# Kernel optimization log

Measured on AMD Instinct MI355X. Metric: run time of the kernel, lower is better.

Reference implementation:

```python
import jax, jax.numpy as jnp
import numpy as np


def _gcn_layer(h, src, dst, W, b, norm_src, norm_dst, n_nodes):
    # DGL GraphConv with norm='both': D_out^{-1/2} -> sum-aggregate -> D_in^{-1/2} -> XW + b
    m = (h * norm_src[:, None])[src]                       # [E, d] gather
    agg = jax.ops.segment_sum(m, dst, num_segments=n_nodes)  # [N, d] scatter-add
    return agg * norm_dst[:, None] @ W + b


def reference(features, src, dst, W1, b1, W2, b2):
    n_nodes = features.shape[0]
    ones = jnp.ones(src.shape[0], dtype=features.dtype)
    deg_out = jax.ops.segment_sum(ones, src, num_segments=n_nodes)
    deg_in = jax.ops.segment_sum(ones, dst, num_segments=n_nodes)
    # DGL clamps degrees to min 1 before the -1/2 power
    norm_src = jnp.clip(deg_out, 1.0, None) ** -0.5
    norm_dst = jnp.clip(deg_in, 1.0, None) ** -0.5

    h = jax.nn.relu(_gcn_layer(features, src, dst, W1, b1, norm_src, norm_dst, n_nodes))
    h = jax.nn.relu(_gcn_layer(h, src, dst, W2, b2, norm_src, norm_dst, n_nodes))
    return h


def setup_inputs() -> dict:
    key = jax.random.key(0)
    k1, k2, k3, k4, k5 = jax.random.split(key, 5)
    N, E, D = 50000, 600000, 128
    scale = 1.0 / np.sqrt(D)
    return {
        "features": jax.random.normal(k1, (N, D), dtype=jnp.float32),
        "src": jax.random.randint(k2, (E,), 0, N, dtype=jnp.int32),
        "dst": jax.random.randint(k3, (E,), 0, N, dtype=jnp.int32),
        "W1": jax.random.normal(k4, (D, D), dtype=jnp.float32) * scale,
        "b1": jnp.zeros((D,), dtype=jnp.float32),
        "W2": jax.random.normal(k5, (D, D), dtype=jnp.float32) * scale,
        "b2": jnp.zeros((D,), dtype=jnp.float32),
    }
```

## Files before the change

### kernel.cpp

```cpp
#include <hip/hip_runtime.h>

#define DIM 128
#define HB  96
#define HWORDS 25088
#define WSTR 136

typedef __attribute__((ext_vector_type(8))) short b8;
typedef __attribute__((ext_vector_type(4))) float f4;
typedef __attribute__((ext_vector_type(8))) unsigned short u16x8;

static __device__ __forceinline__ unsigned short f2bf(float f) {
    unsigned u = __float_as_uint(f);
    u += 0x7fffu + ((u >> 16) & 1u);
    return (unsigned short)(u >> 16);
}
static __device__ __forceinline__ float bf2f(unsigned short b) {
    return __uint_as_float((unsigned)b << 16);
}

__global__ __launch_bounds__(256) void k_hist(const int* __restrict__ src,
                                              const int* __restrict__ dst,
                                              unsigned short* __restrict__ local,
                                              unsigned* __restrict__ hist_in,
                                              unsigned* __restrict__ hist_out,
                                              int E, int W2p, int slice) {
    __shared__ unsigned h[HWORDS];
    const int t = threadIdx.x;
    const int b = blockIdx.x;
    const int e0 = b * slice;
    const int e1 = min(e0 + slice, E);
    const int W4 = W2p >> 2;
    uint4* h4 = (uint4*)h;

    for (int w = t; w < W4; w += 256) h4[w] = make_uint4(0u, 0u, 0u, 0u);
    __syncthreads();
    for (int e = e0 + t; e < e1; e += 256) {
        int d = dst[e];
        unsigned sh = (unsigned)(d & 1) * 16u;
        unsigned old = atomicAdd(&h[d >> 1], 1u << sh);
        local[e] = (unsigned short)((old >> sh) & 0xffffu);
    }
    __syncthreads();
    uint4* oin = (uint4*)(hist_in + (size_t)b * W2p);
    for (int w = t; w < W4; w += 256) { oin[w] = h4[w]; h4[w] = make_uint4(0u, 0u, 0u, 0u); }
    __syncthreads();
    for (int e = e0 + t; e < e1; e += 256) {
        int s = src[e];
        atomicAdd(&h[s >> 1], 1u << ((unsigned)(s & 1) * 16u));
    }
    __syncthreads();
    uint4* oout = (uint4*)(hist_out + (size_t)b * W2p);
    for (int w = t; w < W4; w += 256) oout[w] = h4[w];
}

__global__ __launch_bounds__(256) void k_colscan(unsigned* __restrict__ hist_in,
                                                 const unsigned* __restrict__ hist_out,
                                                 int* __restrict__ cnt,
                                                 int* __restrict__ deg_out,
                                                 int* __restrict__ bsum,
                                                 int W2, int W2p, int N) {
    __shared__ int wsum[4];
    int w = blockIdx.x * 256 + threadIdx.x;
    unsigned run = 0;
    if (w < W2) {
        unsigned* p = hist_in + w;
        #pragma unroll 8
        for (int b = 0; b < HB; ++b) {
            unsigned x = *p;
            *p = run;
            run += x;
            p += W2p;
        }
        unsigned run2 = 0;
        const unsigned* q = hist_out + w;
        #pragma unroll 8
        for (int b = 0; b < HB; ++b) { run2 += *q; q += W2p; }
        int n0 = w * 2;
        if (n0 + 1 < N) {
            *(int2*)(cnt + n0)     = make_int2((int)(run & 0xffffu), (int)(run >> 16));
            *(int2*)(deg_out + n0) = make_int2((int)(run2 & 0xffffu), (int)(run2 >> 16));
        } else {
            cnt[n0]     = (int)(run & 0xffffu);
            deg_out[n0] = (int)(run2 & 0xffffu);
            run &= 0xffffu;
        }
    }
    int tot = (int)(run & 0xffffu) + (int)(run >> 16);
    #pragma unroll
    for (int off = 32; off > 0; off >>= 1) tot += __shfl_down(tot, off, 64);
    int lane = threadIdx.x & 63, wave = threadIdx.x >> 6;
    if (lane == 0) wsum[wave] = tot;
    __syncthreads();
    if (threadIdx.x == 0)   bsum[2 * blockIdx.x]     = wsum[0] + wsum[1];
    if (threadIdx.x == 128) bsum[2 * blockIdx.x + 1] = wsum[2] + wsum[3];
}

__global__ __launch_bounds__(256) void k_edge_pass_fb(const int* __restrict__ src,
                                                      const int* __restrict__ dst,
                                                      int* __restrict__ deg_out,
                                                      int* __restrict__ cnt,
                                                      int* __restrict__ local_fb, int E) {
    int e = blockIdx.x * 256 + threadIdx.x;
    if (e < E) {
        atomicAdd(&deg_out[src[e]], 1);
        local_fb[e] = atomicAdd(&cnt[dst[e]], 1);
    }
}

__global__ __launch_bounds__(256) void k_block_reduce(const int* __restrict__ deg,
                                                      int* __restrict__ bsum, int N) {
    __shared__ int wsum[4];
    int i = blockIdx.x * 256 + threadIdx.x;
    int x = (i < N) ? deg[i] : 0;
    #pragma unroll
    for (int off = 32; off > 0; off >>= 1) x += __shfl_down(x, off, 64);
    int lane = threadIdx.x & 63, wave = threadIdx.x >> 6;
    if (lane == 0) wsum[wave] = x;
    __syncthreads();
    if (threadIdx.x == 0) bsum[blockIdx.x] = wsum[0] + wsum[1] + wsum[2] + wsum[3];
}

__global__ __launch_bounds__(256) void k_scan_final(const int* __restrict__ cnt,
                                                    const int* __restrict__ deg_out,
                                                    const int* __restrict__ bsum,
                                                    int* __restrict__ row_off,
                                                    float* __restrict__ norm_src,
                                                    float* __restrict__ norm_dst, int N) {
    __shared__ int wsum[4];
    __shared__ int base_s;
    const int t = threadIdx.x;
    const int lane = t & 63, wave = t >> 6;

    int pre = 0;
    for (int i = t; i < blockIdx.x; i += 256) pre += bsum[i];
    #pragma unroll
    for (int off = 32; off > 0; off >>= 1) pre += __shfl_down(pre, off, 64);
    if (lane == 0) wsum[wave] = pre;
    __syncthreads();
    if (t == 0) base_s = wsum[0] + wsum[1] + wsum[2] + wsum[3];
    __syncthreads();
    const int bpre_v = base_s;

    int i = blockIdx.x * 256 + t;
    int x = (i < N) ? cnt[i] : 0;
    int orig = x;
    #pragma unroll
    for (int off = 1; off < 64; off <<= 1) {
        int y = __shfl_up(x, off, 64);
        if (lane >= off) x += y;
    }
    if (lane == 63) wsum[wave] = x;
    __syncthreads();
    if (t == 0) {
        int s = 0;
        for (int w = 0; w < 4; ++w) { int tt = wsum[w]; wsum[w] = s; s += tt; }
    }
    __syncthreads();
    x += wsum[wave] + bpre_v;
    if (i < N) {
        row_off[i] = x - orig;
        int di = orig < 1 ? 1 : orig;
        norm_dst[i] = rsqrtf((float)di);
        int dov = deg_out[i]; if (dov < 1) dov = 1;
        norm_src[i] = rsqrtf((float)dov);
    }
    if (i == N - 1) row_off[N] = x;
}

__global__ __launch_bounds__(256) void k_fill_cast_prep(
        const int* __restrict__ src, const int* __restrict__ dst,
        const int* __restrict__ row_off,
        const unsigned short* __restrict__ local,
        const int* __restrict__ local_fb,
        const unsigned* __restrict__ hist_in,
        int* __restrict__ csr_src,
        const float* __restrict__ feat, const float* __restrict__ norm_src,
        unsigned short* __restrict__ fbf,
        const float* __restrict__ W1, const float* __restrict__ W2,
        unsigned short* __restrict__ w1hi, unsigned short* __restrict__ w1lo,
        unsigned short* __restrict__ w2hi, unsigned short* __restrict__ w2lo,
        int E, int W2p, int slice, int eb, int cb, int pb, int n4) {
    int bx = blockIdx.x;
    if (bx < eb) {
        int e = bx * 256 + threadIdx.x;
        if (e < E) {
            int d = dst[e];
            int pos = row_off[d];
            if (hist_in) {
                int b = e / slice;
                unsigned sh = (unsigned)(d & 1) * 16u;
                unsigned bo = (hist_in[(size_t)b * W2p + (d >> 1)] >> sh) & 0xffffu;
                pos += (int)bo + (int)local[e];
            } else {
                pos += local_fb[e];
            }
            csr_src[pos] = src[e];
        }
    } else if (bx < eb + cb) {
        int i = (bx - eb) * 256 + threadIdx.x;
        if (i < n4) {
            float4 v = ((const float4*)feat)[i];
            float ns = norm_src[i >> 5];
            ushort4 o;
            o.x = f2bf(v.x * ns); o.y = f2bf(v.y * ns);
            o.z = f2bf(v.z * ns); o.w = f2bf(v.w * ns);
            ((ushort4*)fbf)[i] = o;
        }
    } else {
        int b = bx - eb - cb;
        const float* W; unsigned short *Hi, *Lo;
        if (b < pb) { W = W1; Hi = w1hi; Lo = w1lo; } else { W = W2; Hi = w2hi; Lo = w2lo; b -= pb; }
        int e = b * 256 + threadIdx.x;
        if (e < DIM * DIM) {
            int k = e >> 7, c = e & 127;
            float w = W[e];
            unsigned short hi = f2bf(w);
            unsigned short lo = f2bf(w - bf2f(hi));
            Hi[c * DIM + k] = hi;
            Lo[c * DIM + k] = lo;
        }
    }
}

__global__ __launch_bounds__(256) void k_spmm(const unsigned short* __restrict__ hb,
                                              const int* __restrict__ csr_src,
                                              const int* __restrict__ row_off,
                                              const float* __restrict__ norm_dst,
                                              unsigned short* __restrict__ aggbf, int N) {
    int t = blockIdx.x * 256 + threadIdx.x;
    int node = t >> 4;
    int lane = t & 15;
    if (node >= N) return;
    int beg = row_off[node], end = row_off[node + 1];
    float a0[8] = {0.f, 0.f, 0.f, 0.f, 0.f, 0.f, 0.f, 0.f};
    float a1[8] = {0.f, 0.f, 0.f, 0.f, 0.f, 0.f, 0.f, 0.f};
    int i = beg;
    for (; i + 4 <= end; i += 4) {
        int s0 = csr_src[i], s1 = csr_src[i + 1], s2 = csr_src[i + 2], s3 = csr_src[i + 3];
        u16x8 u0 = *((const u16x8*)(hb + (size_t)s0 * DIM) + lane);
        u16x8 u1 = *((const u16x8*)(hb + (size_t)s1 * DIM) + lane);
        u16x8 u2 = *((const u16x8*)(hb + (size_t)s2 * DIM) + lane);
        u16x8 u3 = *((const u16x8*)(hb + (size_t)s3 * DIM) + lane);
        #pragma unroll
        for (int j = 0; j < 8; ++j) {
            a0[j] += bf2f(u0[j]);
            a1[j] += bf2f(u1[j]);
            a0[j] += bf2f(u2[j]);
            a1[j] += bf2f(u3[j]);
        }
    }
    for (; i < end; ++i) {
        int s0 = csr_src[i];
        u16x8 u0 = *((const u16x8*)(hb + (size_t)s0 * DIM) + lane);
        #pragma unroll
        for (int j = 0; j < 8; ++j) a0[j] += bf2f(u0[j]);
    }
    float nd = norm_dst[node];
    u16x8 o;
    #pragma unroll
    for (int j = 0; j < 8; ++j) o[j] = f2bf((a0[j] + a1[j]) * nd);
    *((u16x8*)(aggbf + (size_t)node * DIM) + lane) = o;
}

__global__ __launch_bounds__(256, 2) void k_gemm_mfma(
        const unsigned short* __restrict__ A,
        const unsigned short* __restrict__ Wt_hi,
        const unsigned short* __restrict__ Wt_lo,
        const float* __restrict__ bias,
        const float* __restrict__ postscale,
        float* __restrict__ outf, unsigned short* __restrict__ outbf, int N) {
    __shared__ unsigned short WH[DIM * WSTR];
    __shared__ unsigned short WL[DIM * WSTR];

    const int t = threadIdx.x;
    #pragma unroll
    for (int i = 0; i < 8; ++i) {
        int e = (t + i * 256) * 8;
        int c = e >> 7, k = e & 127;
        *(float4*)(WH + c * WSTR + k) = *(const float4*)(Wt_hi + e);
        *(float4*)(WL + c * WSTR + k) = *(const float4*)(Wt_lo + e);
    }
    __syncthreads();

    const int wv = t >> 6;
    const int l = t & 63;
    const int m = l & 15;
    const int quad = l >> 4;
    const int row_t0 = blockIdx.x * 128 + wv * 32;

    f4 acc[2][8];
    #pragma unroll
    for (int rt = 0; rt < 2; ++rt)
        #pragma unroll
        for (int ct = 0; ct < 8; ++ct)
            acc[rt][ct] = (f4){0.f, 0.f, 0.f, 0.f};

    int r0 = row_t0 + m;      if (r0 >= N) r0 = N - 1;
    int r1 = row_t0 + 16 + m; if (r1 >= N) r1 = N - 1;

    #pragma unroll
    for (int ks = 0; ks < 4; ++ks) {
        int koff = ks * 32 + quad * 8;
        b8 a0 = *(const b8*)(A + (size_t)r0 * DIM + koff);
        b8 a1 = *(const b8*)(A + (size_t)r1 * DIM + koff);
        #pragma unroll
        for (int ct = 0; ct < 8; ++ct) {
            int c = ct * 16 + m;
            b8 bh = *(const b8*)(WH + c * WSTR + koff);
            b8 bl = *(const b8*)(WL + c * WSTR + koff);
            acc[0][ct] = __builtin_amdgcn_mfma_f32_16x16x32_bf16(a0, bh, acc[0][ct], 0, 0, 0);
            acc[0][ct] = __builtin_amdgcn_mfma_f32_16x16x32_bf16(a0, bl, acc[0][ct], 0, 0, 0);
            acc[1][ct] = __builtin_amdgcn_mfma_f32_16x16x32_bf16(a1, bh, acc[1][ct], 0, 0, 0);
            acc[1][ct] = __builtin_amdgcn_mfma_f32_16x16x32_bf16(a1, bl, acc[1][ct], 0, 0, 0);
        }
    }

    #pragma unroll
    for (int rt = 0; rt < 2; ++rt) {
        int rowb = row_t0 + rt * 16 + quad * 4;
        #pragma unroll
        for (int r = 0; r < 4; ++r) {
            int gr = rowb + r;
            if (gr < N) {
                float s = postscale ? postscale[gr] : 1.f;
                #pragma unroll
                for (int ct = 0; ct < 8; ++ct) {
                    int col = ct * 16 + m;
                    float v = fmaxf(acc[rt][ct][r] + bias[col], 0.f) * s;
                    if (outbf) outbf[(size_t)gr * DIM + col] = f2bf(v);
                    else       outf[(size_t)gr * DIM + col] = v;
                }
            }
        }
    }
}

static inline size_t align_up(size_t x, size_t a) { return (x + a - 1) & ~(a - 1); }

extern "C" void kernel_launch(void* const* d_in, const int* in_sizes, int n_in,
                              void* d_out, int out_size, void* d_ws, size_t ws_size,
                              hipStream_t stream) {
    const float* features = (const float*)d_in[0];
    const int*   src      = (const int*)d_in[1];
    const int*   dst      = (const int*)d_in[2];
    const float* W1       = (const float*)d_in[3];
    const float* b1       = (const float*)d_in[4];
    const float* W2       = (const float*)d_in[5];
    const float* b2       = (const float*)d_in[6];
    float* out = (float*)d_out;

    const int N = in_sizes[0] / DIM;
    const int E = in_sizes[1];
    const int B = (N + 255) / 256;
    const int W2w = (N + 1) >> 1;
    const int W2p = (W2w + 3) & ~3;
    const int slice = (E + HB - 1) / HB;
    const int cs_blocks = (W2w + 255) / 256;

    size_t nodeb = align_up((size_t)N * 4, 256);
    char* p = (char*)d_ws;
    int*   deg_out  = (int*)p;                      p += nodeb;
    int*   cnt      = (int*)p;                      p += nodeb;
    float* norm_src = (float*)p;                    p += nodeb;
    float* norm_dst = (float*)p;                    p += nodeb;
    int*   row_off  = (int*)p;                      p += align_up((size_t)(N + 1) * 4, 256);
    int*   bsum     = (int*)p;                      p += align_up((size_t)(2 * cs_blocks) * 4, 256);
    int*   csr_src  = (int*)p;                      p += align_up((size_t)E * 4, 256);
    char*  big      = p;                            p += 2 * (size_t)N * DIM * 4;
    unsigned short* w1hi = (unsigned short*)p;      p += (size_t)DIM * DIM * 2;
    unsigned short* w1lo = (unsigned short*)p;      p += (size_t)DIM * DIM * 2;
    unsigned short* w2hi = (unsigned short*)p;      p += (size_t)DIM * DIM * 2;
    unsigned short* w2lo = (unsigned short*)p;      p += (size_t)DIM * DIM * 2;
    unsigned short* aggbf = (unsigned short*)big;
    unsigned short* h1bf  = (unsigned short*)(big + (size_t)N * DIM * 2);
    unsigned short* fbf   = (unsigned short*)(big + 3 * (size_t)N * DIM * 2);
    char* ap = big;
    unsigned short* local = (unsigned short*)ap;    ap += align_up((size_t)E * 2, 256);
    unsigned* hist_in  = (unsigned*)ap;             ap += (size_t)HB * W2p * 4;
    unsigned* hist_out = (unsigned*)ap;             ap += (size_t)HB * W2p * 4;
    int* local_fb = (int*)big;

    const int edge_blocks = (E + 255) / 256;
    const int spmm_blocks = (int)(((size_t)N * 16 + 255) / 256);
    const int gemm_blocks = (N + 127) / 128;
    const int n4 = N * (DIM / 4);
    const int cast_blocks = (n4 + 255) / 256;
    const int prep_blocks = (DIM * DIM + 255) / 256;
    const int fcp_blocks  = edge_blocks + cast_blocks + 2 * prep_blocks;

    const bool fast = (W2p <= HWORDS) &&
        (align_up((size_t)E * 2, 256) + 2 * (size_t)HB * W2p * 4
            <= 3 * (size_t)N * DIM * 2);

    if (fast) {
        k_hist<<<HB, 256, 0, stream>>>(src, dst, local, hist_in, hist_out, E, W2p, slice);
        k_colscan<<<cs_blocks, 256, 0, stream>>>(hist_in, hist_out, cnt, deg_out, bsum, W2w, W2p, N);
        k_scan_final<<<B, 256, 0, stream>>>(cnt, deg_out, bsum, row_off, norm_src, norm_dst, N);
        k_fill_cast_prep<<<fcp_blocks, 256, 0, stream>>>(
            src, dst, row_off, local, (const int*)nullptr, hist_in, csr_src,
            features, norm_src, fbf, W1, W2, w1hi, w1lo, w2hi, w2lo,
            E, W2p, slice, edge_blocks, cast_blocks, prep_blocks, n4);
    } else {
        hipMemsetAsync(deg_out, 0, nodeb * 2, stream);
        k_edge_pass_fb<<<edge_blocks, 256, 0, stream>>>(src, dst, deg_out, cnt, local_fb, E);
        k_block_reduce<<<B, 256, 0, stream>>>(cnt, bsum, N);
        k_scan_final<<<B, 256, 0, stream>>>(cnt, deg_out, bsum, row_off, norm_src, norm_dst, N);
        k_fill_cast_prep<<<fcp_blocks, 256, 0, stream>>>(
            src, dst, row_off, (const unsigned short*)nullptr, local_fb,
            (const unsigned*)nullptr, csr_src,
            features, norm_src, fbf, W1, W2, w1hi, w1lo, w2hi, w2lo,
            E, W2p, slice, edge_blocks, cast_blocks, prep_blocks, n4);
    }

    k_spmm<<<spmm_blocks, 256, 0, stream>>>(fbf, csr_src, row_off, norm_dst, aggbf, N);
    k_gemm_mfma<<<gemm_blocks, 256, 0, stream>>>(aggbf, w1hi, w1lo, b1, norm_src,
                                                 (float*)nullptr, h1bf, N);

    k_spmm<<<spmm_blocks, 256, 0, stream>>>(h1bf, csr_src, row_off, norm_dst, aggbf, N);
    k_gemm_mfma<<<gemm_blocks, 256, 0, stream>>>(aggbf, w2hi, w2lo, b2, (const float*)nullptr,
                                                 out, (unsigned short*)nullptr, N);
}
```

Baseline: 226.3 us.

## Split histogram kernel into separate dst and src blocks with 1024 threads

The histogram kernel previously had each of 96 blocks count both dst and src degrees in sequence. It now launches 64 blocks for dst and 64 for src, each with 1024 threads, and prefetches the next index before each LDS atomic. The aim is more parallelism and better latency hiding in this setup stage on the 256-CU part, at the cost of each block zeroing and writing out a full LDS histogram. The fill kernel now gets slice_d so its local-offset lookup stays consistent with the dst partition.

```diff
diff --git a/kernel.cpp b/kernel.cpp
--- a/kernel.cpp
+++ b/kernel.cpp
@@ -1,7 +1,8 @@
 #include <hip/hip_runtime.h>
 
 #define DIM 128
-#define HB  96
+#define HBD 64
+#define HBS 64
 #define HWORDS 25088
 #define WSTR 136
 
@@ -18,39 +19,50 @@
     return __uint_as_float((unsigned)b << 16);
 }
 
-__global__ __launch_bounds__(256) void k_hist(const int* __restrict__ src,
-                                              const int* __restrict__ dst,
-                                              unsigned short* __restrict__ local,
-                                              unsigned* __restrict__ hist_in,
-                                              unsigned* __restrict__ hist_out,
-                                              int E, int W2p, int slice) {
+__global__ __launch_bounds__(1024) void k_hist(const int* __restrict__ src,
+                                               const int* __restrict__ dst,
+                                               unsigned short* __restrict__ local,
+                                               unsigned* __restrict__ hist_in,
+                                               unsigned* __restrict__ hist_out,
+                                               int E, int W2p, int slice_d, int slice_s) {
     __shared__ unsigned h[HWORDS];
     const int t = threadIdx.x;
-    const int b = blockIdx.x;
+    const bool is_dst = blockIdx.x < HBD;
+    const int b = is_dst ? blockIdx.x : blockIdx.x - HBD;
+    const int slice = is_dst ? slice_d : slice_s;
     const int e0 = b * slice;
     const int e1 = min(e0 + slice, E);
     const int W4 = W2p >> 2;
     uint4* h4 = (uint4*)h;
 
-    for (int w = t; w < W4; w += 256) h4[w] = make_uint4(0u, 0u, 0u, 0u);
-    __syncthreads();
-    for (int e = e0 + t; e < e1; e += 256) {
-        int d = dst[e];
-        unsigned sh = (unsigned)(d & 1) * 16u;
-        unsigned old = atomicAdd(&h[d >> 1], 1u << sh);
-        local[e] = (unsigned short)((old >> sh) & 0xffffu);
-    }
-    __syncthreads();
-    uint4* oin = (uint4*)(hist_in + (size_t)b * W2p);
-    for (int w = t; w < W4; w += 256) { oin[w] = h4[w]; h4[w] = make_uint4(0u, 0u, 0u, 0u); }
-    __syncthreads();
-    for (int e = e0 + t; e < e1; e += 256) {
-        int s = src[e];
-        atomicAdd(&h[s >> 1], 1u << ((unsigned)(s & 1) * 16u));
-    }
-    __syncthreads();
-    uint4* oout = (uint4*)(hist_out + (size_t)b * W2p);
-    for (int w = t; w < W4; w += 256) oout[w] = h4[w];
+    for (int w = t; w < W4; w += 1024) h4[w] = make_uint4(0u, 0u, 0u, 0u);
+    __syncthreads();
+
+    if (is_dst) {
+        int e = e0 + t;
+        int d = (e < e1) ? dst[e] : 0;
+        while (e < e1) {
+            int en = e + 1024;
+            int dn = (en < e1) ? dst[en] : 0;
+            unsigned sh = (unsigned)(d & 1) * 16u;
+            unsigned old = atomicAdd(&h[d >> 1], 1u << sh);
+            local[e] = (unsigned short)((old >> sh) & 0xffffu);
+            e = en; d = dn;
+        }
+    } else {
+        int e = e0 + t;
+        int s = (e < e1) ? src[e] : 0;
+        while (e < e1) {
+            int en = e + 1024;
+            int sn = (en < e1) ? src[en] : 0;
+            atomicAdd(&h[s >> 1], 1u << ((unsigned)(s & 1) * 16u));
+            e = en; s = sn;
+        }
+    }
+    __syncthreads();
+
+    uint4* o = (uint4*)((is_dst ? hist_in : hist_out) + (size_t)b * W2p);
+    for (int w = t; w < W4; w += 1024) o[w] = h4[w];
 }
 
 __global__ __launch_bounds__(256) void k_colscan(unsigned* __restrict__ hist_in,
@@ -65,7 +77,7 @@
     if (w < W2) {
         unsigned* p = hist_in + w;
         #pragma unroll 8
-        for (int b = 0; b < HB; ++b) {
+        for (int b = 0; b < HBD; ++b) {
             unsigned x = *p;
             *p = run;
             run += x;
@@ -74,7 +86,7 @@
         unsigned run2 = 0;
         const unsigned* q = hist_out + w;
         #pragma unroll 8
-        for (int b = 0; b < HB; ++b) { run2 += *q; q += W2p; }
+        for (int b = 0; b < HBS; ++b) { run2 += *q; q += W2p; }
         int n0 = w * 2;
         if (n0 + 1 < N) {
             *(int2*)(cnt + n0)     = make_int2((int)(run & 0xffffu), (int)(run >> 16));
@@ -354,7 +366,8 @@
     const int B = (N + 255) / 256;
     const int W2w = (N + 1) >> 1;
     const int W2p = (W2w + 3) & ~3;
-    const int slice = (E + HB - 1) / HB;
+    const int slice_d = (E + HBD - 1) / HBD;
+    const int slice_s = (E + HBS - 1) / HBS;
     const int cs_blocks = (W2w + 255) / 256;
 
     size_t nodeb = align_up((size_t)N * 4, 256);
@@ -376,8 +389,8 @@
     unsigned short* fbf   = (unsigned short*)(big + 3 * (size_t)N * DIM * 2);
     char* ap = big;
     unsigned short* local = (unsigned short*)ap;    ap += align_up((size_t)E * 2, 256);
-    unsigned* hist_in  = (unsigned*)ap;             ap += (size_t)HB * W2p * 4;
-    unsigned* hist_out = (unsigned*)ap;             ap += (size_t)HB * W2p * 4;
+    unsigned* hist_in  = (unsigned*)ap;             ap += (size_t)HBD * W2p * 4;
+    unsigned* hist_out = (unsigned*)ap;             ap += (size_t)HBS * W2p * 4;
     int* local_fb = (int*)big;
 
     const int edge_blocks = (E + 255) / 256;
@@ -389,17 +402,18 @@
     const int fcp_blocks  = edge_blocks + cast_blocks + 2 * prep_blocks;
 
     const bool fast = (W2p <= HWORDS) &&
-        (align_up((size_t)E * 2, 256) + 2 * (size_t)HB * W2p * 4
+        (align_up((size_t)E * 2, 256) + (size_t)(HBD + HBS) * W2p * 4
             <= 3 * (size_t)N * DIM * 2);
 
     if (fast) {
-        k_hist<<<HB, 256, 0, stream>>>(src, dst, local, hist_in, hist_out, E, W2p, slice);
+        k_hist<<<HBD + HBS, 1024, 0, stream>>>(src, dst, local, hist_in, hist_out,
+                                               E, W2p, slice_d, slice_s);
         k_colscan<<<cs_blocks, 256, 0, stream>>>(hist_in, hist_out, cnt, deg_out, bsum, W2w, W2p, N);
         k_scan_final<<<B, 256, 0, stream>>>(cnt, deg_out, bsum, row_off, norm_src, norm_dst, N);
         k_fill_cast_prep<<<fcp_blocks, 256, 0, stream>>>(
             src, dst, row_off, local, (const int*)nullptr, hist_in, csr_src,
             features, norm_src, fbf, W1, W2, w1hi, w1lo, w2hi, w2lo,
-            E, W2p, slice, edge_blocks, cast_blocks, prep_blocks, n4);
+            E, W2p, slice_d, edge_blocks, cast_blocks, prep_blocks, n4);
     } else {
         hipMemsetAsync(deg_out, 0, nodeb * 2, stream);
         k_edge_pass_fb<<<edge_blocks, 256, 0, stream>>>(src, dst, deg_out, cnt, local_fb, E);
@@ -409,7 +423,7 @@
             src, dst, row_off, (const unsigned short*)nullptr, local_fb,
             (const unsigned*)nullptr, csr_src,
             features, norm_src, fbf, W1, W2, w1hi, w1lo, w2hi, w2lo,
-            E, W2p, slice, edge_blocks, cast_blocks, prep_blocks, n4);
+            E, W2p, slice_d, edge_blocks, cast_blocks, prep_blocks, n4);
     }
 
     k_spmm<<<spmm_blocks, 256, 0, stream>>>(fbf, csr_src, row_off, norm_dst, aggbf, N);
```

Measured after the change: 207.4 us, median of 2. 1.09x faster.
